# Performance work log

Measured on AMD Instinct MI355X. Metric: run time of the kernel, lower is better.

## Reference

```python
import jax, jax.numpy as jnp
import numpy as np

B, S, D, H = 2, 4096, 256, 4
DH = D // H  # 64


def setup_inputs() -> dict:
    key = jax.random.key(0)
    ks = jax.random.split(key, 7)
    scale = 1.0 / np.sqrt(DH)  # torch Linear default init range ~ U(-1/sqrt(in), 1/sqrt(in))
    def w(k):
        return jax.random.uniform(k, (H, DH, DH), jnp.float32, -scale, scale)
    def b(k):
        return jax.random.uniform(k, (H, DH), jnp.float32, -scale, scale)
    return {
        "sequences": jax.random.normal(ks[0], (B, S, D), jnp.float32),
        "qw": w(ks[1]), "qb": b(ks[2]),
        "kw": w(ks[3]), "kb": b(ks[4]),
        "vw": w(ks[5]), "vb": b(ks[6]),
        "train": 0,
    }


def reference(sequences, qw, qb, kw, kb, vw, vb, train):
    # sequences: [B, S, D] -> per-head slices [B, H, S, DH]
    x = sequences.reshape(B, S, H, DH).transpose(0, 2, 1, 3)  # [B,H,S,DH]
    # torch Linear: y = x @ W.T + b, W: [out, in]
    q = jnp.einsum('bhsd,hed->bhse', x, qw) + qb[None, :, None, :]
    k = jnp.einsum('bhsd,hed->bhse', x, kw) + kb[None, :, None, :]
    v = jnp.einsum('bhsd,hed->bhse', x, vw) + vb[None, :, None, :]
    scores = jnp.einsum('bhqd,bhkd->bhqk', q, k) / jnp.sqrt(jnp.float32(DH))
    attn = jax.nn.softmax(scores, axis=-1)  # [B,H,S,S]
    out = jnp.einsum('bhqk,bhkd->bhqd', attn, v)  # [B,H,S,DH]
    # hstack over heads == concatenate head outputs along feature dim
    return out.transpose(0, 2, 1, 3).reshape(B, S, D)
```

## Files before the change

### kernel.cpp

```cpp
#include <hip/hip_runtime.h>
#include <hip/hip_bf16.h>


#define B_   2
#define S_   4096
#define D_   256
#define H_   4
#define DH_  64
#define BH_  8
#define NTOK (BH_*S_*DH_)

#define KVB  64
#define QW   32
#define NW   8
#define QB   (QW*NW)
#define NINST (BH_*(S_/QW))

typedef short v8s __attribute__((ext_vector_type(8)));
typedef float v16f __attribute__((ext_vector_type(16)));
typedef float v4f __attribute__((ext_vector_type(4)));
typedef unsigned v4u __attribute__((ext_vector_type(4)));
typedef unsigned v2u __attribute__((ext_vector_type(2)));
typedef int v2i __attribute__((ext_vector_type(2)));

#define QSCL (0.125f * 1.4426950408889634f)
#define DEFER_THR 8.0f

static __device__ __forceinline__ short f2bf(float f) {
    __hip_bfloat16 h = __float2bfloat16(f);
    return *reinterpret_cast<short*>(&h);
}
static __device__ __forceinline__ unsigned cvtpk(float lo, float hi) {
    unsigned r;
    asm("v_cvt_pk_bf16_f32 %0, %1, %2" : "=v"(r) : "v"(lo), "v"(hi));
    return r;
}
static __device__ __forceinline__ float fexp2(float x) {
#if __has_builtin(__builtin_amdgcn_exp2f)
    return __builtin_amdgcn_exp2f(x);
#else
    float r;
    asm("v_exp_f32 %0, %1" : "=v"(r) : "v"(x));
    return r;
#endif
}
static __device__ __forceinline__ float max3f(float a, float b, float c) {
    return fmaxf(fmaxf(a, b), c);
}
static __device__ __forceinline__ void pl32swap(unsigned &a, unsigned &b) {
#if __has_builtin(__builtin_amdgcn_permlane32_swap)
    v2i r = __builtin_amdgcn_permlane32_swap((int)a, (int)b, false, false);
    a = (unsigned)r[0]; b = (unsigned)r[1];
#else
    asm volatile("v_permlane32_swap_b32 %0, %1" : "+v"(a), "+v"(b));
#endif
}
static __device__ __forceinline__ void gl2lds(const short* g, short* l) {
    __builtin_amdgcn_global_load_lds(
        (const __attribute__((address_space(1))) void*)g,
        (__attribute__((address_space(3))) void*)l, 16, 0, 0);
}
static __device__ __forceinline__ v16f vz16() {
    v16f z;
    #pragma unroll
    for (int i = 0; i < 16; ++i) z[i] = 0.f;
    return z;
}
static __device__ __forceinline__ v8s cvt8(const float* p) {
    v4f f0 = *(const v4f*)(p);
    v4f f1 = *(const v4f*)(p + 4);
    v4u u = { cvtpk(f0[0], f0[1]), cvtpk(f0[2], f0[3]),
              cvtpk(f1[0], f1[1]), cvtpk(f1[2], f1[3]) };
    return __builtin_bit_cast(v8s, u);
}

__global__ __launch_bounds__(128) void qkv_proj_mfma(
    const float* __restrict__ x,
    const float* __restrict__ qw, const float* __restrict__ qb,
    const float* __restrict__ kw, const float* __restrict__ kb,
    const float* __restrict__ vw, const float* __restrict__ vb,
    short* __restrict__ Qo, short* __restrict__ Ko, short* __restrict__ Vt)
{
    const int t   = threadIdx.x;
    const int w   = t >> 6;
    const int l   = t & 63;
    const int l31 = l & 31, lhi = l >> 5;
    const int bh  = blockIdx.y, h = bh & 3, b = bh >> 2;
    const int s0  = blockIdx.x * 32;

    const float* xrow = x + ((size_t)(b*S_ + s0 + l31))*D_ + h*DH_;
    v8s af[4];
    #pragma unroll
    for (int k0 = 0; k0 < 4; ++k0)
        af[k0] = cvt8(xrow + k0*16 + lhi*8);

    const float* Wp[3] = { qw + h*DH_*DH_, kw + h*DH_*DH_, vw + h*DH_*DH_ };
    const float* Bp[3] = { qb + h*DH_,     kb + h*DH_,     vb + h*DH_ };
    short* Qh = Qo + (size_t)bh*S_*DH_;
    short* Kh = Ko + (size_t)bh*S_*DH_;

    #pragma unroll
    for (int ui = 0; ui < 3; ++ui) {
        const int u  = w*3 + ui;
        const int p  = u >> 1;
        const int eb = u & 1;
        const int e  = eb*32 + l31;
        const float* wrow = Wp[p] + e*DH_;

        v16f acc = vz16();
        #pragma unroll
        for (int k0 = 0; k0 < 4; ++k0) {
            v8s bfr = cvt8(wrow + k0*16 + lhi*8);
            acc = __builtin_amdgcn_mfma_f32_32x32x16_bf16(af[k0], bfr, acc, 0, 0, 0);
        }

        const float bias = Bp[p][e];
        if (p == 0) {
            const float bq = bias * QSCL;
            #pragma unroll
            for (int r = 0; r < 16; ++r) acc[r] = fmaf(acc[r], QSCL, bq);
        } else {
            #pragma unroll
            for (int r = 0; r < 16; ++r) acc[r] += bias;
        }

        if (p < 2) {
            short* dst = (p == 0) ? Qh : Kh;
            #pragma unroll
            for (int r = 0; r < 16; ++r) {
                int s = s0 + (r & 3) + 8*(r >> 2) + 4*lhi;
                dst[(size_t)s*DH_ + e] = f2bf(acc[r]);
            }
        } else {
            short* vtb = Vt + (size_t)bh*DH_*S_ + (size_t)e*S_;
            #pragma unroll
            for (int rq = 0; rq < 4; ++rq) {
                v2u pr = { cvtpk(acc[rq*4+0], acc[rq*4+1]),
                           cvtpk(acc[rq*4+2], acc[rq*4+3]) };
                int s = s0 + rq*8 + 4*lhi;
                *(v2u*)(vtb + s) = pr;
            }
        }
    }
}

__global__ __launch_bounds__(512, 4) void attn_kernel(
    const short* __restrict__ Q, const short* __restrict__ K,
    const short* __restrict__ Vt, float* __restrict__ Opart,
    float* __restrict__ Ml, int nspl, int kvlen)
{
    __shared__ __align__(16) short klds[4][64][64];
    __shared__ __align__(16) short vlds[4][64][64];

    const int t    = threadIdx.x;
    const int w    = t >> 6;
    const int l    = t & 63;
    const int l31  = l & 31;
    const int lhi  = l >> 5;
    const int bh   = blockIdx.y;
    const int qtil = blockIdx.x;
    const int spl  = blockIdx.z;
    const int q0   = qtil*QB + w*QW;
    const int kv_beg = spl * kvlen;

    const short* Qh = Q  + (size_t)bh*S_*DH_;
    const short* Kh = K  + (size_t)bh*S_*DH_;
    const short* Vh = Vt + (size_t)bh*DH_*S_;

    const int rl  = l >> 3;
    const int cs  = (l & 7) ^ (rl & 7);
    const size_t koff = (size_t)(w*8 + rl)*DH_ + cs*8;
    const size_t voff = (size_t)(w*8 + rl)*S_  + cs*8;
    short* kls = (short*)klds + w*512;
    short* vls = (short*)vlds + w*512;

    v8s qf[4];
    #pragma unroll
    for (int k0 = 0; k0 < 4; ++k0)
        qf[k0] = *(const v8s*)(Qh + (size_t)(q0 + l31)*DH_ + k0*16 + lhi*8);

    int fo[2][4];
    #pragma unroll
    for (int a = 0; a < 2; ++a)
        #pragma unroll
        for (int c = 0; c < 4; ++c)
            fo[a][c] = (a*32 + l31)*64 + (((c*2 + lhi) ^ (l31 & 7))*8);

    v16f o0 = vz16(), o1 = vz16();
    float m_run = -INFINITY, l_run = 0.f;

    const int NT = kvlen / KVB;

    auto stage = [&](int tile, int buf) {
        const size_t kvo = kv_beg + (size_t)tile*KVB;
        gl2lds(Kh + kvo*DH_ + koff, kls + buf*4096);
        gl2lds(Vh + kvo      + voff, vls + buf*4096);
    };

    auto tilebody = [&](int buf) {
        const short* kb = (const short*)klds + buf*4096;
        const short* vb = (const short*)vlds + buf*4096;

        v16f s0 = vz16(), s1 = vz16();
        __builtin_amdgcn_s_setprio(1);
        #pragma unroll
        for (int k0 = 0; k0 < 4; ++k0) {
            v8s a0 = *(const v8s*)(kb + fo[0][k0]);
            v8s a1 = *(const v8s*)(kb + fo[1][k0]);
            s0 = __builtin_amdgcn_mfma_f32_32x32x16_bf16(a0, qf[k0], s0, 0, 0, 0);
            s1 = __builtin_amdgcn_mfma_f32_32x32x16_bf16(a1, qf[k0], s1, 0, 0, 0);
        }
        __builtin_amdgcn_s_setprio(0);

        float t16[16];
        #pragma unroll
        for (int i = 0; i < 16; ++i) t16[i] = fmaxf(s0[i], s1[i]);
        float r0 = max3f(t16[0],  t16[1],  t16[2]);
        float r1 = max3f(t16[3],  t16[4],  t16[5]);
        float r2 = max3f(t16[6],  t16[7],  t16[8]);
        float r3 = max3f(t16[9],  t16[10], t16[11]);
        float r4 = max3f(t16[12], t16[13], t16[14]);
        float mx = fmaxf(max3f(max3f(r0, r1, r2), r3, r4), t16[15]);
        mx = fmaxf(mx, __shfl_xor(mx, 32));

        if (__any(mx > m_run + DEFER_THR)) {
            float mn = fmaxf(m_run, mx);
            float sc = fexp2(m_run - mn);
            #pragma unroll
            for (int i = 0; i < 16; ++i) { o0[i] *= sc; o1[i] *= sc; }
            l_run *= sc;
            m_run = mn;
        }
        #pragma unroll
        for (int i = 0; i < 16; ++i) s0[i] = fexp2(s0[i] - m_run);
        #pragma unroll
        for (int i = 0; i < 16; ++i) s1[i] = fexp2(s1[i] - m_run);
        float a16[16];
        #pragma unroll
        for (int i = 0; i < 16; ++i) a16[i] = s0[i] + s1[i];
        #pragma unroll
        for (int st = 8; st; st >>= 1)
            #pragma unroll
            for (int i = 0; i < st; ++i) a16[i] += a16[i+st];
        l_run += a16[0] + __shfl_xor(a16[0], 32);

        unsigned pwv[4][4];
        {
            unsigned j0 = cvtpk(s0[0], s0[1]),  j1 = cvtpk(s0[2], s0[3]);
            unsigned j2 = cvtpk(s0[4], s0[5]),  j3 = cvtpk(s0[6], s0[7]);
            unsigned j4 = cvtpk(s0[8], s0[9]),  j5 = cvtpk(s0[10], s0[11]);
            unsigned j6 = cvtpk(s0[12], s0[13]), j7 = cvtpk(s0[14], s0[15]);
            pl32swap(j0, j2); pl32swap(j1, j3);
            pwv[0][0] = j0; pwv[0][1] = j1; pwv[0][2] = j2; pwv[0][3] = j3;
            pl32swap(j4, j6); pl32swap(j5, j7);
            pwv[1][0] = j4; pwv[1][1] = j5; pwv[1][2] = j6; pwv[1][3] = j7;
        }
        {
            unsigned j0 = cvtpk(s1[0], s1[1]),  j1 = cvtpk(s1[2], s1[3]);
            unsigned j2 = cvtpk(s1[4], s1[5]),  j3 = cvtpk(s1[6], s1[7]);
            unsigned j4 = cvtpk(s1[8], s1[9]),  j5 = cvtpk(s1[10], s1[11]);
            unsigned j6 = cvtpk(s1[12], s1[13]), j7 = cvtpk(s1[14], s1[15]);
            pl32swap(j0, j2); pl32swap(j1, j3);
            pwv[2][0] = j0; pwv[2][1] = j1; pwv[2][2] = j2; pwv[2][3] = j3;
            pl32swap(j4, j6); pl32swap(j5, j7);
            pwv[3][0] = j4; pwv[3][1] = j5; pwv[3][2] = j6; pwv[3][3] = j7;
        }

        __builtin_amdgcn_s_setprio(1);
        #pragma unroll
        for (int kk = 0; kk < 4; ++kk) {
            v4u u = { pwv[kk][0], pwv[kk][1], pwv[kk][2], pwv[kk][3] };
            v8s pf = __builtin_bit_cast(v8s, u);
            v8s va0 = *(const v8s*)(vb + fo[0][kk]);
            v8s va1 = *(const v8s*)(vb + fo[1][kk]);
            o0 = __builtin_amdgcn_mfma_f32_32x32x16_bf16(va0, pf, o0, 0, 0, 0);
            o1 = __builtin_amdgcn_mfma_f32_32x32x16_bf16(va1, pf, o1, 0, 0, 0);
        }
        __builtin_amdgcn_s_setprio(0);
    };

    stage(0, 0);
    stage(1, 1);
    __syncthreads();

    for (int it = 0; it < NT; it += 2) {
        if (it + 2 < NT) stage(it + 2, (it + 2) & 3);
        tilebody(it & 3);
        if (it + 3 < NT) stage(it + 3, (it + 3) & 3);
        tilebody((it + 1) & 3);
        __syncthreads();
    }

    const int inst = bh*(S_/QW) + qtil*NW + w;
    float* od = Opart + ((size_t)inst*nspl + spl)*2048;
    #pragma unroll
    for (int r = 0; r < 16; ++r) od[r*64 + l]      = o0[r];
    #pragma unroll
    for (int r = 0; r < 16; ++r) od[(16+r)*64 + l] = o1[r];
    Ml[((size_t)inst*nspl + spl)*64 + l] = (l < 32) ? m_run : l_run;
}

template<int NSPL>
__global__ __launch_bounds__(256) void combine_kernel(
    const float* __restrict__ Opart, const float* __restrict__ Ml,
    float* __restrict__ out)
{
    const int t = threadIdx.x;
    const int w = t >> 6, l = t & 63;
    const int inst = blockIdx.x*4 + w;
    const int bh = inst >> 7;
    const int qw = inst & 127;
    const int b = bh >> 2, h = bh & 3;
    const int l31 = l & 31, lhi = l >> 5;
    const int q = qw*32 + l31;

    const float* mlp = Ml + (size_t)inst*NSPL*64;
    float m[NSPL], lv[NSPL];
    float M = -INFINITY;
    #pragma unroll
    for (int sp = 0; sp < NSPL; ++sp) {
        m[sp]  = mlp[sp*64 + l31];
        lv[sp] = mlp[sp*64 + 32 + l31];
        M = fmaxf(M, m[sp]);
    }
    float wgt[NSPL], L = 0.f;
    #pragma unroll
    for (int sp = 0; sp < NSPL; ++sp) {
        wgt[sp] = fexp2(m[sp] - M);
        L += lv[sp] * wgt[sp];
    }
    float inv = 1.f / L;

    const float* op0 = Opart + (size_t)inst*NSPL*2048;
    float* outp = out + ((size_t)(b*S_ + q))*D_ + h*DH_;

    #pragma unroll
    for (int g = 0; g < 8; ++g) {
        v4f acc;
        #pragma unroll
        for (int jj = 0; jj < 4; ++jj) {
            int r = g*4 + jj;
            float v = 0.f;
            #pragma unroll
            for (int sp = 0; sp < NSPL; ++sp)
                v += op0[sp*2048 + r*64 + l] * wgt[sp];
            acc[jj] = v * inv;
        }
        int td = g >> 2, gg = g & 3;
        int d = td*32 + gg*8 + lhi*4;
        *(v4f*)(outp + d) = acc;
    }
}

extern "C" void kernel_launch(void* const* d_in, const int* in_sizes, int n_in,
                              void* d_out, int out_size, void* d_ws, size_t ws_size,
                              hipStream_t stream)
{
    const float* x  = (const float*)d_in[0];
    const float* qw = (const float*)d_in[1];
    const float* qb = (const float*)d_in[2];
    const float* kw = (const float*)d_in[3];
    const float* kb = (const float*)d_in[4];
    const float* vw = (const float*)d_in[5];
    const float* vb = (const float*)d_in[6];

    short* Qb  = (short*)d_ws;
    short* Kb  = Qb + NTOK;
    short* Vtb = Kb + NTOK;
    float* Opart = (float*)(Vtb + NTOK);

    size_t base = (size_t)3*NTOK*sizeof(short);
    size_t per_spl = (size_t)NINST*2048*4 + (size_t)NINST*64*4;
    int nspl = 1;
    if      (ws_size >= base + 4*per_spl) nspl = 4;
    else if (ws_size >= base + 2*per_spl) nspl = 2;
    float* Ml = Opart + (size_t)NINST*nspl*2048;
    int kvlen = S_/nspl;

    float* out = (float*)d_out;

    dim3 pg(S_/32, BH_), pb(128);
    hipLaunchKernelGGL(qkv_proj_mfma, pg, pb, 0, stream,
                       x, qw, qb, kw, kb, vw, vb, Qb, Kb, Vtb);

    dim3 ag(S_/QB, BH_, nspl), ab(512);
    hipLaunchKernelGGL(attn_kernel, ag, ab, 0, stream, Qb, Kb, Vtb, Opart, Ml, nspl, kvlen);

    dim3 cg(NINST/4), cb(256);
    if (nspl == 4)
        hipLaunchKernelGGL(combine_kernel<4>, cg, cb, 0, stream, Opart, Ml, out);
    else if (nspl == 2)
        hipLaunchKernelGGL(combine_kernel<2>, cg, cb, 0, stream, Opart, Ml, out);
    else
        hipLaunchKernelGGL(combine_kernel<1>, cg, cb, 0, stream, Opart, Ml, out);
}
```

Measured before the change: 73.98 us.

## Replace direct global-to-LDS quad-buffering with register-staged double buffering; allow 8 KV splits

The attention kernel stops using global_load_lds into a 4-deep LDS ring. It now loads the next K/V tile into registers during the current tile's compute, writes it into the other half of a 2-deep LDS buffer, and syncs every tile. This halves LDS use, which could raise occupancy, but it adds a barrier per tile and register pressure. Separately, the host can pick 8 KV splits when the workspace allows, giving more blocks but more partial outputs for the combine kernel to read.

Result: slower. 88.60 us (+19.8%).

```diff
diff --git a/kernel.cpp b/kernel.cpp
--- a/kernel.cpp
+++ b/kernel.cpp
@@ -54,11 +54,6 @@
 #else
     asm volatile("v_permlane32_swap_b32 %0, %1" : "+v"(a), "+v"(b));
 #endif
-}
-static __device__ __forceinline__ void gl2lds(const short* g, short* l) {
-    __builtin_amdgcn_global_load_lds(
-        (const __attribute__((address_space(1))) void*)g,
-        (__attribute__((address_space(3))) void*)l, 16, 0, 0);
 }
 static __device__ __forceinline__ v16f vz16() {
     v16f z;
@@ -149,8 +144,8 @@
     const short* __restrict__ Vt, float* __restrict__ Opart,
     float* __restrict__ Ml, int nspl, int kvlen)
 {
-    __shared__ __align__(16) short klds[4][64][64];
-    __shared__ __align__(16) short vlds[4][64][64];
+    __shared__ __align__(16) short klds[2][64][64];
+    __shared__ __align__(16) short vlds[2][64][64];
 
     const int t    = threadIdx.x;
     const int w    = t >> 6;
@@ -171,8 +166,7 @@
     const int cs  = (l & 7) ^ (rl & 7);
     const size_t koff = (size_t)(w*8 + rl)*DH_ + cs*8;
     const size_t voff = (size_t)(w*8 + rl)*S_  + cs*8;
-    short* kls = (short*)klds + w*512;
-    short* vls = (short*)vlds + w*512;
+    const int ldst = w*512 + l*8;
 
     v8s qf[4];
     #pragma unroll
@@ -191,15 +185,26 @@
 
     const int NT = kvlen / KVB;
 
-    auto stage = [&](int tile, int buf) {
-        const size_t kvo = kv_beg + (size_t)tile*KVB;
-        gl2lds(Kh + kvo*DH_ + koff, kls + buf*4096);
-        gl2lds(Vh + kvo      + voff, vls + buf*4096);
-    };
-
-    auto tilebody = [&](int buf) {
-        const short* kb = (const short*)klds + buf*4096;
-        const short* vb = (const short*)vlds + buf*4096;
+    {
+        v8s k0v = *(const v8s*)(Kh + (size_t)kv_beg*DH_ + koff);
+        v8s v0v = *(const v8s*)(Vh + kv_beg + voff);
+        *(v8s*)((short*)klds[0] + ldst) = k0v;
+        *(v8s*)((short*)vlds[0] + ldst) = v0v;
+    }
+    __syncthreads();
+
+    for (int it = 0; it < NT; ++it) {
+        const int cur = it & 1;
+
+        v8s knx, vnx;
+        if (it + 1 < NT) {
+            size_t kvn = kv_beg + (size_t)(it+1)*KVB;
+            knx = *(const v8s*)(Kh + kvn*DH_ + koff);
+            vnx = *(const v8s*)(Vh + kvn + voff);
+        }
+
+        const short* kb = (const short*)klds[cur];
+        const short* vb = (const short*)vlds[cur];
 
         v16f s0 = vz16(), s1 = vz16();
         __builtin_amdgcn_s_setprio(1);
@@ -277,17 +282,11 @@
             o1 = __builtin_amdgcn_mfma_f32_32x32x16_bf16(va1, pf, o1, 0, 0, 0);
         }
         __builtin_amdgcn_s_setprio(0);
-    };
-
-    stage(0, 0);
-    stage(1, 1);
-    __syncthreads();
-
-    for (int it = 0; it < NT; it += 2) {
-        if (it + 2 < NT) stage(it + 2, (it + 2) & 3);
-        tilebody(it & 3);
-        if (it + 3 < NT) stage(it + 3, (it + 3) & 3);
-        tilebody((it + 1) & 3);
+
+        if (it + 1 < NT) {
+            *(v8s*)((short*)klds[cur^1] + ldst) = knx;
+            *(v8s*)((short*)vlds[cur^1] + ldst) = vnx;
+        }
         __syncthreads();
     }
 
@@ -372,7 +371,8 @@
     size_t base = (size_t)3*NTOK*sizeof(short);
     size_t per_spl = (size_t)NINST*2048*4 + (size_t)NINST*64*4;
     int nspl = 1;
-    if      (ws_size >= base + 4*per_spl) nspl = 4;
+    if      (ws_size >= base + 8*per_spl) nspl = 8;
+    else if (ws_size >= base + 4*per_spl) nspl = 4;
     else if (ws_size >= base + 2*per_spl) nspl = 2;
     float* Ml = Opart + (size_t)NINST*nspl*2048;
     int kvlen = S_/nspl;
@@ -387,7 +387,9 @@
     hipLaunchKernelGGL(attn_kernel, ag, ab, 0, stream, Qb, Kb, Vtb, Opart, Ml, nspl, kvlen);
 
     dim3 cg(NINST/4), cb(256);
-    if (nspl == 4)
+    if (nspl == 8)
+        hipLaunchKernelGGL(combine_kernel<8>, cg, cb, 0, stream, Opart, Ml, out);
+    else if (nspl == 4)
         hipLaunchKernelGGL(combine_kernel<4>, cg, cb, 0, stream, Opart, Ml, out);
     else if (nspl == 2)
         hipLaunchKernelGGL(combine_kernel<2>, cg, cb, 0, stream, Opart, Ml, out);
```

## Replace global_load_lds with register-staged K/V prefetch and permlane32 reductions

Applied to the files above, without the earlier changes.

K/V tiles were loaded with direct global-to-LDS loads. They now go through registers: each load is issued before the tile's compute and written to LDS after it, so global latency is hidden behind the MFMA work. The cross-half max and sum reductions also switch from __shfl_xor (a ds_bpermute through LDS) to v_permlane32_swap. The register staging raises VGPR pressure and adds LDS write instructions, which could hurt occupancy or issue rate.

Result: no change. 74.23 us (+0.3%).

```diff
diff --git a/kernel.cpp b/kernel.cpp
--- a/kernel.cpp
+++ b/kernel.cpp
@@ -55,10 +55,15 @@
     asm volatile("v_permlane32_swap_b32 %0, %1" : "+v"(a), "+v"(b));
 #endif
 }
-static __device__ __forceinline__ void gl2lds(const short* g, short* l) {
-    __builtin_amdgcn_global_load_lds(
-        (const __attribute__((address_space(1))) void*)g,
-        (__attribute__((address_space(3))) void*)l, 16, 0, 0);
+static __device__ __forceinline__ float xmax32(float x) {
+    unsigned a = __builtin_bit_cast(unsigned, x), b = a;
+    pl32swap(a, b);
+    return fmaxf(__builtin_bit_cast(float, a), __builtin_bit_cast(float, b));
+}
+static __device__ __forceinline__ float xadd32(float x) {
+    unsigned a = __builtin_bit_cast(unsigned, x), b = a;
+    pl32swap(a, b);
+    return __builtin_bit_cast(float, a) + __builtin_bit_cast(float, b);
 }
 static __device__ __forceinline__ v16f vz16() {
     v16f z;
@@ -171,8 +176,7 @@
     const int cs  = (l & 7) ^ (rl & 7);
     const size_t koff = (size_t)(w*8 + rl)*DH_ + cs*8;
     const size_t voff = (size_t)(w*8 + rl)*S_  + cs*8;
-    short* kls = (short*)klds + w*512;
-    short* vls = (short*)vlds + w*512;
+    const int ldst = w*512 + l*8;
 
     v8s qf[4];
     #pragma unroll
@@ -191,10 +195,12 @@
 
     const int NT = kvlen / KVB;
 
-    auto stage = [&](int tile, int buf) {
+    auto stage_direct = [&](int tile, int buf) {
         const size_t kvo = kv_beg + (size_t)tile*KVB;
-        gl2lds(Kh + kvo*DH_ + koff, kls + buf*4096);
-        gl2lds(Vh + kvo      + voff, vls + buf*4096);
+        v8s kv = *(const v8s*)(Kh + kvo*DH_ + koff);
+        v8s vv = *(const v8s*)(Vh + kvo      + voff);
+        *(v8s*)((short*)klds + buf*4096 + ldst) = kv;
+        *(v8s*)((short*)vlds + buf*4096 + ldst) = vv;
     };
 
     auto tilebody = [&](int buf) {
@@ -221,7 +227,7 @@
         float r3 = max3f(t16[9],  t16[10], t16[11]);
         float r4 = max3f(t16[12], t16[13], t16[14]);
         float mx = fmaxf(max3f(max3f(r0, r1, r2), r3, r4), t16[15]);
-        mx = fmaxf(mx, __shfl_xor(mx, 32));
+        mx = xmax32(mx);
 
         if (__any(mx > m_run + DEFER_THR)) {
             float mn = fmaxf(m_run, mx);
@@ -242,7 +248,7 @@
         for (int st = 8; st; st >>= 1)
             #pragma unroll
             for (int i = 0; i < st; ++i) a16[i] += a16[i+st];
-        l_run += a16[0] + __shfl_xor(a16[0], 32);
+        l_run += xadd32(a16[0]);
 
         unsigned pwv[4][4];
         {
@@ -279,15 +285,33 @@
         __builtin_amdgcn_s_setprio(0);
     };
 
-    stage(0, 0);
-    stage(1, 1);
+    stage_direct(0, 0);
+    stage_direct(1, 1);
     __syncthreads();
 
     for (int it = 0; it < NT; it += 2) {
-        if (it + 2 < NT) stage(it + 2, (it + 2) & 3);
+        v8s k2, v2;
+        if (it + 2 < NT) {
+            size_t kvn = kv_beg + (size_t)(it+2)*KVB;
+            k2 = *(const v8s*)(Kh + kvn*DH_ + koff);
+            v2 = *(const v8s*)(Vh + kvn + voff);
+        }
         tilebody(it & 3);
-        if (it + 3 < NT) stage(it + 3, (it + 3) & 3);
+        if (it + 2 < NT) {
+            *(v8s*)((short*)klds + ((it+2)&3)*4096 + ldst) = k2;
+            *(v8s*)((short*)vlds + ((it+2)&3)*4096 + ldst) = v2;
+        }
+        v8s k3, v3;
+        if (it + 3 < NT) {
+            size_t kvn = kv_beg + (size_t)(it+3)*KVB;
+            k3 = *(const v8s*)(Kh + kvn*DH_ + koff);
+            v3 = *(const v8s*)(Vh + kvn + voff);
+        }
         tilebody((it + 1) & 3);
+        if (it + 3 < NT) {
+            *(v8s*)((short*)klds + ((it+3)&3)*4096 + ldst) = k3;
+            *(v8s*)((short*)vlds + ((it+3)&3)*4096 + ldst) = v3;
+        }
         __syncthreads();
     }
 
```
